# Optimization experiments

Hardware: AMD Instinct MI355X
Metric: run time of the kernel (lower is better)

Reference implementation:

```python
import jax, jax.numpy as jnp
import numpy as np

N = 50000
E = 800000
D = 128


def _gcn_layer(x, row, col, ew, W, b, n):
    # PyG GCNConv (normalize=True, add_self_loops=True):
    # self-loops were already appended to row/col/ew by the caller.
    deg = jax.ops.segment_sum(ew, col, num_segments=n)          # [N]
    dis = jnp.where(deg > 0, jax.lax.rsqrt(jnp.maximum(deg, 1e-12)), 0.0)
    norm = dis[row] * ew * dis[col]                              # [E+N]
    h = x @ W                                                    # [N, D]
    msg = h[row] * norm[:, None]                                 # [E+N, D] gather-scale
    out = jax.ops.segment_sum(msg, col, num_segments=n)          # scatter-add
    return out + b


def setup_inputs() -> dict:
    key = jax.random.key(0)
    k1, k2, k3, k4, k5 = jax.random.split(key, 5)
    x = jax.random.normal(k1, (N, D), dtype=jnp.float32)
    edge_index = jax.random.randint(k2, (2, E), 0, N, dtype=jnp.int64)
    edge_weight = jax.random.uniform(k3, (E,), dtype=jnp.float32)
    s = 1.0 / np.sqrt(D)
    W1 = jax.random.uniform(k4, (D, D), minval=-s, maxval=s, dtype=jnp.float32)
    b1 = jnp.zeros((D,), dtype=jnp.float32)
    W2 = jax.random.uniform(k5, (D, D), minval=-s, maxval=s, dtype=jnp.float32)
    b2 = jnp.zeros((D,), dtype=jnp.float32)
    return {"x": x, "edge_index": edge_index, "edge_weight": edge_weight,
            "W1": W1, "b1": b1, "W2": W2, "b2": b2}


def reference(x, edge_index, edge_weight, W1, b1, W2, b2):
    n = x.shape[0]
    loop = jnp.arange(n, dtype=edge_index.dtype)
    row = jnp.concatenate([edge_index[0], loop])
    col = jnp.concatenate([edge_index[1], loop])
    ew = jnp.concatenate([edge_weight, jnp.ones((n,), dtype=edge_weight.dtype)])
    h = _gcn_layer(x, row, col, ew, W1, b1, n)
    h = jax.nn.relu(h)
    # F.dropout(training=self.training): identity in eval mode
    out = _gcn_layer(h, row, col, ew, W2, b2, n)
    return out
```

## Files before the change

kernel.cpp:

```cpp
#include <hip/hip_runtime.h>

#define NN 50000
#define NE 800000
#define DD 128

#define CAP 64
#define QPAD 8
#define FIX_SCALE 16777216.0f
#define LOW40 ((1ULL << 40) - 1)
#define NWELEM 16384

typedef __attribute__((ext_vector_type(8))) short short8;
typedef __attribute__((ext_vector_type(4))) float floatx4;
typedef __attribute__((ext_vector_type(4))) _Float16 half4;
typedef __attribute__((ext_vector_type(8))) _Float16 half8;


__device__ __forceinline__ void split_trunc(float x, short& hi, short& lo) {
    unsigned uh = __float_as_uint(x) >> 16;
    hi = (short)uh;
    float r = x - __uint_as_float(uh << 16);
    lo = (short)(__float_as_uint(r) >> 16);
}


__global__ void init_prep(unsigned long long* __restrict__ cursor64,
                          const float* __restrict__ W1, const float* __restrict__ W2,
                          unsigned short* __restrict__ w1hi, unsigned short* __restrict__ w1lo,
                          unsigned short* __restrict__ w2hi, unsigned short* __restrict__ w2lo) {
    int t = blockIdx.x * blockDim.x + threadIdx.x;
    if (t < NN) cursor64[t * QPAD] = 0ULL;
    int u = t - NN;
    if (u >= 0 && u < 2 * NWELEM) {
        int which = u >> 14;
        int idx = u & (NWELEM - 1);
        int k = idx >> 7, n = idx & 127;
        const float* W = which ? W2 : W1;
        unsigned short* whi = which ? w2hi : w1hi;
        unsigned short* wlo = which ? w2lo : w1lo;
        short h, l;
        split_trunc(W[idx], h, l);
        whi[n * DD + k] = (unsigned short)h;
        wlo[n * DD + k] = (unsigned short)l;
    }
}


__global__ void place_direct(const int* __restrict__ row, const int* __restrict__ col,
                             const float* __restrict__ ew,
                             unsigned long long* __restrict__ cursor64,
                             uint2* __restrict__ epk) {
    int e = blockIdx.x * blockDim.x + threadIdx.x;
    if (e >= NE) return;
    int c = col[e];
    float w = ew[e];
    unsigned q = (unsigned)(w * FIX_SCALE + 0.5f);
    unsigned long long old = atomicAdd(&cursor64[c * QPAD], (1ULL << 40) | (unsigned long long)q);
    int rank = (int)(old >> 40);
    uint2 p;
    p.x = (unsigned)(row[e] * DD);
    p.y = __float_as_uint(w);
    epk[(c << 6) + rank] = p;
}

__global__ void node_dis(const unsigned long long* __restrict__ cursor64,
                         float* __restrict__ dis, int* __restrict__ endarr) {
    int i = blockIdx.x * blockDim.x + threadIdx.x;
    if (i >= NN) return;
    unsigned long long cv = cursor64[i * QPAD];
    int cnt = (int)(cv >> 40);
    float deg = 1.0f + (float)(cv & LOW40) * (1.0f / FIX_SCALE);
    dis[i] = rsqrtf(deg);
    endarr[i] = (i << 6) + cnt;
}


template <bool RELU, typename InT>
__global__ __launch_bounds__(256, 2) void gemm_mfma(const InT* __restrict__ in,
                                                    const unsigned short* __restrict__ whi,
                                                    const unsigned short* __restrict__ wlo,
                                                    const float* __restrict__ dis,
                                                    _Float16* __restrict__ out) {
    int lane = threadIdx.x & 63;
    int wid = threadIdx.x >> 6;
    int cg = wid & 1;
    int rg = wid >> 1;
    int l16 = lane & 15;
    int quad = lane >> 4;
    int koff_base = quad * 8;

    short8 bhi[4][4], blo[4][4];
#pragma unroll
    for (int t = 0; t < 4; t++) {
        int n = cg * 64 + t * 16 + l16;
#pragma unroll
        for (int ks = 0; ks < 4; ks++) {
            int koff = ks * 32 + koff_base;
            bhi[t][ks] = *(const short8*)(whi + n * DD + koff);
            blo[t][ks] = *(const short8*)(wlo + n * DD + koff);
        }
    }

#pragma unroll
    for (int chunk = 0; chunk < 4; chunk++) {
        int base = blockIdx.x * 128 + chunk * 32 + rg * 16;
        int m = base + l16;
        int mld = (m < NN) ? m : 0;
        const InT* xr = in + (size_t)mld * DD;

        short8 ahi[4], alo[4];
#pragma unroll
        for (int ks = 0; ks < 4; ks++) {
            int koff = ks * 32 + koff_base;
            float v[8];
            if constexpr (sizeof(InT) == 4) {
                float4 a0 = *(const float4*)(xr + koff);
                float4 a1 = *(const float4*)(xr + koff + 4);
                v[0] = a0.x; v[1] = a0.y; v[2] = a0.z; v[3] = a0.w;
                v[4] = a1.x; v[5] = a1.y; v[6] = a1.z; v[7] = a1.w;
            } else {
                half8 a = *(const half8*)(xr + koff);
#pragma unroll
                for (int j = 0; j < 8; j++) v[j] = (float)a[j];
            }
#pragma unroll
            for (int j = 0; j < 8; j++) {
                float xv = RELU ? fmaxf(v[j], 0.0f) : v[j];
                short h, l;
                split_trunc(xv, h, l);
                ahi[ks][j] = h;
                alo[ks][j] = l;
            }
        }

        floatx4 acc[4];
#pragma unroll
        for (int t = 0; t < 4; t++) acc[t] = (floatx4)(0.0f);

#pragma unroll
        for (int ks = 0; ks < 4; ks++) {
#pragma unroll
            for (int t = 0; t < 4; t++) {
                acc[t] = __builtin_amdgcn_mfma_f32_16x16x32_bf16(ahi[ks], bhi[t][ks], acc[t], 0, 0, 0);
                acc[t] = __builtin_amdgcn_mfma_f32_16x16x32_bf16(alo[ks], bhi[t][ks], acc[t], 0, 0, 0);
                acc[t] = __builtin_amdgcn_mfma_f32_16x16x32_bf16(ahi[ks], blo[t][ks], acc[t], 0, 0, 0);
            }
        }

#pragma unroll
        for (int r = 0; r < 4; r++) {
            int rowm = base + quad * 4 + r;
            if (rowm < NN) {
                float dsc = dis[rowm];
                _Float16* o = out + (size_t)rowm * DD + cg * 64 + l16;
#pragma unroll
                for (int t = 0; t < 4; t++) o[t * 16] = (_Float16)(acc[t][r] * dsc);
            }
        }
    }
}


template <typename OutT>
__global__ __launch_bounds__(256) void agg_half(const int* __restrict__ endarr,
                                                const uint2* __restrict__ epk,
                                                const _Float16* __restrict__ g,
                                                const float* __restrict__ dis,
                                                const float* __restrict__ bias,
                                                OutT* __restrict__ out) {
    int i = (blockIdx.x * blockDim.x + threadIdx.x) >> 6;
    int lane = threadIdx.x & 63;
    int s = lane & 31;
    int half = lane >> 5;
    if (i >= NN) return;

    half4 gv = *(const half4*)(g + (size_t)i * DD + s * 4);
    float4 bb = ((const float4*)bias)[s];
    float d = dis[i];

    float ax = 0.0f, ay = 0.0f, az = 0.0f, aw = 0.0f;

    int start = i << 6;
    int end = endarr[i];
    int j = start + half;
    for (; j + 6 < end; j += 8) {
        uint2 p0 = epk[j], p1 = epk[j + 2], p2 = epk[j + 4], p3 = epk[j + 6];
        half4 v0 = *(const half4*)(g + p0.x + s * 4);
        half4 v1 = *(const half4*)(g + p1.x + s * 4);
        half4 v2 = *(const half4*)(g + p2.x + s * 4);
        half4 v3 = *(const half4*)(g + p3.x + s * 4);
        float n0 = __uint_as_float(p0.y), n1 = __uint_as_float(p1.y);
        float n2 = __uint_as_float(p2.y), n3 = __uint_as_float(p3.y);
        ax = fmaf(n0, (float)v0.x, ax); ay = fmaf(n0, (float)v0.y, ay);
        az = fmaf(n0, (float)v0.z, az); aw = fmaf(n0, (float)v0.w, aw);
        ax = fmaf(n1, (float)v1.x, ax); ay = fmaf(n1, (float)v1.y, ay);
        az = fmaf(n1, (float)v1.z, az); aw = fmaf(n1, (float)v1.w, aw);
        ax = fmaf(n2, (float)v2.x, ax); ay = fmaf(n2, (float)v2.y, ay);
        az = fmaf(n2, (float)v2.z, az); aw = fmaf(n2, (float)v2.w, aw);
        ax = fmaf(n3, (float)v3.x, ax); ay = fmaf(n3, (float)v3.y, ay);
        az = fmaf(n3, (float)v3.z, az); aw = fmaf(n3, (float)v3.w, aw);
    }
    for (; j < end; j += 2) {
        uint2 p = epk[j];
        float nm = __uint_as_float(p.y);
        half4 v = *(const half4*)(g + p.x + s * 4);
        ax = fmaf(nm, (float)v.x, ax); ay = fmaf(nm, (float)v.y, ay);
        az = fmaf(nm, (float)v.z, az); aw = fmaf(nm, (float)v.w, aw);
    }

    ax += __shfl_xor(ax, 32);
    ay += __shfl_xor(ay, 32);
    az += __shfl_xor(az, 32);
    aw += __shfl_xor(aw, 32);

    if (half == 0) {
        float ox = bb.x + d * (ax + (float)gv.x);
        float oy = bb.y + d * (ay + (float)gv.y);
        float oz = bb.z + d * (az + (float)gv.z);
        float ow = bb.w + d * (aw + (float)gv.w);
        if constexpr (sizeof(OutT) == 2) {
            half4 o;
            o.x = (_Float16)ox; o.y = (_Float16)oy;
            o.z = (_Float16)oz; o.w = (_Float16)ow;
            *(half4*)(out + (size_t)i * DD + s * 4) = o;
        } else {
            float4 o;
            o.x = ox; o.y = oy; o.z = oz; o.w = ow;
            ((float4*)(out + (size_t)i * DD))[s] = o;
        }
    }
}


extern "C" void kernel_launch(void* const* d_in, const int* in_sizes, int n_in,
                              void* d_out, int out_size, void* d_ws, size_t ws_size,
                              hipStream_t stream) {
    const float* x  = (const float*)d_in[0];
    const int*   ei = (const int*)d_in[1];
    const float* ew = (const float*)d_in[2];
    const float* W1 = (const float*)d_in[3];
    const float* b1 = (const float*)d_in[4];
    const float* W2 = (const float*)d_in[5];
    const float* b2 = (const float*)d_in[6];
    float* out = (float*)d_out;

    float* ws      = (float*)d_ws;
    float* dis     = ws;
    int*   endarr  = (int*)(ws + 50000);
    unsigned long long* cursor64 = (unsigned long long*)(ws + 100000);
    uint2* epk     = (uint2*)(ws + 900000);
    _Float16* gbuf = (_Float16*)(ws + 7300000);
    unsigned short* wt1hi = (unsigned short*)(ws + 10500000);
    unsigned short* wt1lo = (unsigned short*)(ws + 10508192);
    unsigned short* wt2hi = (unsigned short*)(ws + 10516384);
    unsigned short* wt2lo = (unsigned short*)(ws + 10524576);
    _Float16* out1 = (_Float16*)(ws + 10532768);

    const int* rowi = ei;
    const int* coli = ei + NE;

    init_prep<<<(NN + 2 * NWELEM + 255) / 256, 256, 0, stream>>>(
        cursor64, W1, W2, wt1hi, wt1lo, wt2hi, wt2lo);
    place_direct<<<(NE + 255) / 256, 256, 0, stream>>>(rowi, coli, ew, cursor64, epk);
    node_dis<<<(NN + 255) / 256, 256, 0, stream>>>(cursor64, dis, endarr);

    const int gemm_grid = (NN + 127) / 128;
    const int agg_grid  = (NN * 64) / 256 + 1;

    gemm_mfma<false, float><<<gemm_grid, 256, 0, stream>>>(x, wt1hi, wt1lo, dis, gbuf);
    agg_half<_Float16><<<agg_grid, 256, 0, stream>>>(endarr, epk, gbuf, dis, b1, out1);

    gemm_mfma<true, _Float16><<<gemm_grid, 256, 0, stream>>>(out1, wt2hi, wt2lo, dis, gbuf);
    agg_half<float><<<agg_grid, 256, 0, stream>>>(endarr, epk, gbuf, dis, b2, out);
}
```

Measured before the change: 259.8 us.

## Co-schedule first GEMM with edge placement and apply degree scale afterward

The first GEMM no longer depends on the degree normalization. It is launched in the same grid as the edge-placement atomics, so the GEMM's compute-bound blocks and the placement's atomic/memory-bound blocks run side by side. A new node_dis_scale kernel computes dis and endarr and rescales the half-precision GEMM output in place, which adds an extra read-write pass over the 50000x128 buffer. The bucket rank is also clamped to CAP to guard against overflow, and removing the separate launches cuts launch overhead.

```diff
diff --git a/kernel.cpp b/kernel.cpp
--- a/kernel.cpp
+++ b/kernel.cpp
@@ -9,6 +9,8 @@
 #define FIX_SCALE 16777216.0f
 #define LOW40 ((1ULL << 40) - 1)
 #define NWELEM 16384
+#define GEMM_GRID ((NN + 127) / 128)
+#define PLACE_GRID ((NE + 255) / 256)
 
 typedef __attribute__((ext_vector_type(8))) short short8;
 typedef __attribute__((ext_vector_type(4))) float floatx4;
@@ -46,41 +48,12 @@
 }
 
 
-__global__ void place_direct(const int* __restrict__ row, const int* __restrict__ col,
-                             const float* __restrict__ ew,
-                             unsigned long long* __restrict__ cursor64,
-                             uint2* __restrict__ epk) {
-    int e = blockIdx.x * blockDim.x + threadIdx.x;
-    if (e >= NE) return;
-    int c = col[e];
-    float w = ew[e];
-    unsigned q = (unsigned)(w * FIX_SCALE + 0.5f);
-    unsigned long long old = atomicAdd(&cursor64[c * QPAD], (1ULL << 40) | (unsigned long long)q);
-    int rank = (int)(old >> 40);
-    uint2 p;
-    p.x = (unsigned)(row[e] * DD);
-    p.y = __float_as_uint(w);
-    epk[(c << 6) + rank] = p;
-}
-
-__global__ void node_dis(const unsigned long long* __restrict__ cursor64,
-                         float* __restrict__ dis, int* __restrict__ endarr) {
-    int i = blockIdx.x * blockDim.x + threadIdx.x;
-    if (i >= NN) return;
-    unsigned long long cv = cursor64[i * QPAD];
-    int cnt = (int)(cv >> 40);
-    float deg = 1.0f + (float)(cv & LOW40) * (1.0f / FIX_SCALE);
-    dis[i] = rsqrtf(deg);
-    endarr[i] = (i << 6) + cnt;
-}
-
-
-template <bool RELU, typename InT>
-__global__ __launch_bounds__(256, 2) void gemm_mfma(const InT* __restrict__ in,
-                                                    const unsigned short* __restrict__ whi,
-                                                    const unsigned short* __restrict__ wlo,
-                                                    const float* __restrict__ dis,
-                                                    _Float16* __restrict__ out) {
+template <bool RELU, bool SCALE, typename InT>
+__device__ __forceinline__ void gemm_core(int bid, const InT* __restrict__ in,
+                                          const unsigned short* __restrict__ whi,
+                                          const unsigned short* __restrict__ wlo,
+                                          const float* __restrict__ dis,
+                                          _Float16* __restrict__ out) {
     int lane = threadIdx.x & 63;
     int wid = threadIdx.x >> 6;
     int cg = wid & 1;
@@ -103,7 +76,7 @@
 
 #pragma unroll
     for (int chunk = 0; chunk < 4; chunk++) {
-        int base = blockIdx.x * 128 + chunk * 32 + rg * 16;
+        int base = bid * 128 + chunk * 32 + rg * 16;
         int m = base + l16;
         int mld = (m < NN) ? m : 0;
         const InT* xr = in + (size_t)mld * DD;
@@ -151,13 +124,79 @@
         for (int r = 0; r < 4; r++) {
             int rowm = base + quad * 4 + r;
             if (rowm < NN) {
-                float dsc = dis[rowm];
+                float dsc = SCALE ? dis[rowm] : 1.0f;
                 _Float16* o = out + (size_t)rowm * DD + cg * 64 + l16;
 #pragma unroll
                 for (int t = 0; t < 4; t++) o[t * 16] = (_Float16)(acc[t][r] * dsc);
             }
         }
     }
+}
+
+
+__device__ __forceinline__ void place_core(int e, const int* __restrict__ row,
+                                           const int* __restrict__ col,
+                                           const float* __restrict__ ew,
+                                           unsigned long long* __restrict__ cursor64,
+                                           uint2* __restrict__ epk) {
+    if (e >= NE) return;
+    int c = col[e];
+    float w = ew[e];
+    unsigned q = (unsigned)(w * FIX_SCALE + 0.5f);
+    unsigned long long old = atomicAdd(&cursor64[c * QPAD], (1ULL << 40) | (unsigned long long)q);
+    int rank = min((int)(old >> 40), CAP - 1);
+    uint2 p;
+    p.x = (unsigned)(row[e] * DD);
+    p.y = __float_as_uint(w);
+    epk[(c << 6) + rank] = p;
+}
+
+
+__global__ __launch_bounds__(256) void gemm1_place(const float* __restrict__ x,
+                                                   const unsigned short* __restrict__ w1hi,
+                                                   const unsigned short* __restrict__ w1lo,
+                                                   _Float16* __restrict__ g,
+                                                   const int* __restrict__ row,
+                                                   const int* __restrict__ col,
+                                                   const float* __restrict__ ew,
+                                                   unsigned long long* __restrict__ cursor64,
+                                                   uint2* __restrict__ epk) {
+    if (blockIdx.x < GEMM_GRID) {
+        gemm_core<false, false, float>(blockIdx.x, x, w1hi, w1lo, nullptr, g);
+    } else {
+        int e = (blockIdx.x - GEMM_GRID) * 256 + threadIdx.x;
+        place_core(e, row, col, ew, cursor64, epk);
+    }
+}
+
+__global__ __launch_bounds__(256, 2) void gemm2(const _Float16* __restrict__ in,
+                                                const unsigned short* __restrict__ whi,
+                                                const unsigned short* __restrict__ wlo,
+                                                const float* __restrict__ dis,
+                                                _Float16* __restrict__ out) {
+    gemm_core<true, true, _Float16>(blockIdx.x, in, whi, wlo, dis, out);
+}
+
+
+__global__ __launch_bounds__(256) void node_dis_scale(const unsigned long long* __restrict__ cursor64,
+                                                      float* __restrict__ dis,
+                                                      int* __restrict__ endarr,
+                                                      _Float16* __restrict__ g) {
+    int t = blockIdx.x * blockDim.x + threadIdx.x;
+    int i = t >> 4, sub = t & 15;
+    if (i >= NN) return;
+    unsigned long long cv = cursor64[i * QPAD];
+    float deg = 1.0f + (float)(cv & LOW40) * (1.0f / FIX_SCALE);
+    float d = rsqrtf(deg);
+    if (sub == 0) {
+        dis[i] = d;
+        endarr[i] = (i << 6) + min((int)(cv >> 40), CAP);
+    }
+    half8* gp = (half8*)(g + (size_t)i * DD + sub * 8);
+    half8 v = *gp;
+#pragma unroll
+    for (int j = 0; j < 8; j++) v[j] = (_Float16)((float)v[j] * d);
+    *gp = v;
 }
 
 
@@ -261,15 +300,17 @@
 
     init_prep<<<(NN + 2 * NWELEM + 255) / 256, 256, 0, stream>>>(
         cursor64, W1, W2, wt1hi, wt1lo, wt2hi, wt2lo);
-    place_direct<<<(NE + 255) / 256, 256, 0, stream>>>(rowi, coli, ew, cursor64, epk);
-    node_dis<<<(NN + 255) / 256, 256, 0, stream>>>(cursor64, dis, endarr);
-
-    const int gemm_grid = (NN + 127) / 128;
-    const int agg_grid  = (NN * 64) / 256 + 1;
-
-    gemm_mfma<false, float><<<gemm_grid, 256, 0, stream>>>(x, wt1hi, wt1lo, dis, gbuf);
+
+    gemm1_place<<<GEMM_GRID + PLACE_GRID, 256, 0, stream>>>(
+        x, wt1hi, wt1lo, gbuf, rowi, coli, ew, cursor64, epk);
+
+    node_dis_scale<<<(NN * 16) / 256, 256, 0, stream>>>(cursor64, dis, endarr, gbuf);
+
+    const int agg_grid = (NN * 64) / 256 + 1;
+
     agg_half<_Float16><<<agg_grid, 256, 0, stream>>>(endarr, epk, gbuf, dis, b1, out1);
 
-    gemm_mfma<true, _Float16><<<gemm_grid, 256, 0, stream>>>(out1, wt2hi, wt2lo, dis, gbuf);
+    gemm2<<<GEMM_GRID, 256, 0, stream>>>(out1, wt2hi, wt2lo, dis, gbuf);
+
     agg_half<float><<<agg_grid, 256, 0, stream>>>(endarr, epk, gbuf, dis, b2, out);
 }
```

New measurement: 231.2 us. -11.0%, faster.
